# Kernel optimization log

Hardware: AMD Instinct MI355X
Metric: run time of the kernel (lower is better)

Reference implementation:

```python
import jax, jax.numpy as jnp
import numpy as np

NUM_ITER = 3  # routing iterations (canonical CapsNet)
EPS = 1e-12


def _conv(x, w, stride):
    return jax.lax.conv_general_dilated(
        x, w, (stride, stride), 'VALID',
        dimension_numbers=('NCHW', 'OIHW', 'NCHW'))


def _squash(t, axis=-1):
    sn = (t * t).sum(axis=axis, keepdims=True)
    return sn / (1.0 + sn) * t / jnp.sqrt(sn + EPS)


def _batchnorm(x, eps=1e-5):
    # fresh BatchNorm2d in training mode: batch stats, weight=1, bias=0, biased var
    m = x.mean((0, 2, 3), keepdims=True)
    v = ((x - m) ** 2).mean((0, 2, 3), keepdims=True)
    return (x - m) * jax.lax.rsqrt(v + eps)


def _branch(x, cw, cb, pw, pb, rw):
    # x: [B,1,H,W]; cw: [128,1,k,k]; pw: [8,32,128,k,k]; rw: [10,R,8,16]
    y = jax.nn.relu(_conv(x, cw, 1) + cb[None, :, None, None])
    y = _batchnorm(y)
    nc, oc = pw.shape[0], pw.shape[1]  # 8 capsules, 32 channels each
    p = _conv(y, pw.reshape(nc * oc, pw.shape[2], pw.shape[3], pw.shape[4]), 2)
    p = p + pb.reshape(-1)[None, :, None, None]          # [B,256,h,w]
    B = p.shape[0]
    u = jnp.transpose(p.reshape(B, nc, -1), (0, 2, 1))   # [B,R,8], R=32*h*w
    u = _squash(u, axis=-1)
    priors = jnp.einsum('bri,nrio->nbro', u, rw)         # [10,B,R,16]
    b = jnp.zeros(priors.shape[:3] + (1,), priors.dtype)  # [10,B,R,1]
    for i in range(NUM_ITER):
        c = jax.nn.softmax(b, axis=2)                    # over route nodes
        v = _squash((c * priors).sum(axis=2, keepdims=True))  # [10,B,1,16]
        if i < NUM_ITER - 1:
            b = b + (priors * v).sum(axis=-1, keepdims=True)
    v = jnp.transpose(v[:, :, 0, :], (1, 0, 2))          # [B,10,16]
    return jnp.sqrt((v * v).sum(-1) + EPS)               # [B,10] capsule lengths


def setup_inputs() -> dict:
    key = jax.random.key(0)
    ks = jax.random.split(key, 16)
    s = 0.05
    return {
        'x': jax.random.normal(ks[0], (256, 1, 28, 28), jnp.float32),
        'conv1_w': jax.random.normal(ks[1], (128, 1, 3, 3), jnp.float32) * s,
        'conv1_b': jnp.zeros((128,), jnp.float32),
        'prim1_w': jax.random.normal(ks[2], (8, 32, 128, 3, 3), jnp.float32) * s,
        'prim1_b': jnp.zeros((8, 32), jnp.float32),
        'digit1_w': jax.random.normal(ks[3], (10, 128, 8, 16), jnp.float32),
        'conv2_w': jax.random.normal(ks[4], (128, 1, 5, 5), jnp.float32) * s,
        'conv2_b': jnp.zeros((128,), jnp.float32),
        'prim2_w': jax.random.normal(ks[5], (8, 32, 128, 5, 5), jnp.float32) * s,
        'prim2_b': jnp.zeros((8, 32), jnp.float32),
        'digit2_w': jax.random.normal(ks[6], (10, 288, 8, 16), jnp.float32),
        'conv3_w': jax.random.normal(ks[7], (128, 1, 9, 9), jnp.float32) * s,
        'conv3_b': jnp.zeros((128,), jnp.float32),
        'prim3_w': jax.random.normal(ks[8], (8, 32, 128, 9, 9), jnp.float32) * s,
        'prim3_b': jnp.zeros((8, 32), jnp.float32),
        'digit3_w': jax.random.normal(ks[9], (10, 1152, 8, 16), jnp.float32),
    }


def reference(x, conv1_w, conv1_b, prim1_w, prim1_b, digit1_w,
              conv2_w, conv2_b, prim2_w, prim2_b, digit2_w,
              conv3_w, conv3_b, prim3_w, prim3_b, digit3_w):
    img = x[:, 0]                                   # [B,28,28]
    B = img.shape[0]
    x3 = img                                        # 28x28
    x2 = img.reshape(B, 14, 2, 14, 2).mean((2, 4))  # 14x14 pyramid level
    x1 = x2.reshape(B, 7, 2, 7, 2).mean((2, 4))     # 7x7 pyramid level
    l1 = _branch(x1[:, None], conv1_w, conv1_b, prim1_w, prim1_b, digit1_w)
    l2 = _branch(x2[:, None], conv2_w, conv2_b, prim2_w, prim2_b, digit2_w)
    l3 = _branch(x3[:, None], conv3_w, conv3_b, prim3_w, prim3_b, digit3_w)
    return jax.nn.softmax(l1 + l2 + l3, axis=-1)    # [B,10]
```

## Files before the change

### kernel.cpp

```cpp
#include <hip/hip_runtime.h>
#include <math.h>

#define SQ_EPS 1e-12f
#define BN_EPS 1e-5f

typedef short short8 __attribute__((ext_vector_type(8)));
typedef float f32x4 __attribute__((ext_vector_type(4)));
typedef unsigned short ushort_t;

__device__ inline unsigned short f2bf(float x) {
    unsigned int u = __float_as_uint(x);
    unsigned int r = (u + 0x7fffu + ((u >> 16) & 1u)) >> 16;
    return (unsigned short)r;
}
__device__ inline float bf2f(unsigned short h) {
    return __uint_as_float(((unsigned int)h) << 16);
}

template<int IH, int IW, int KS, int OH, int OW>
__device__ void conv_body(const float* __restrict__ w, const float* __restrict__ bias,
                          ushort_t* __restrict__ yh, ushort_t* __restrict__ yl,
                          float* __restrict__ partial,
                          int b, int tid, float* s_img, float* s_w, float* s_red) {
    constexpr int KK = KS * KS;
    constexpr int OS = OH * OW;
    for (int i = tid; i < 128 * KK; i += 256) s_w[i] = w[i];
    __syncthreads();
    int c = tid & 127, half = tid >> 7;
    float bias_c = bias[c];
    float bsum = 0.f, bsq = 0.f;
    for (int r = half; r < OH; r += 2) {
        float acc[OW];
        #pragma unroll
        for (int j = 0; j < OW; ++j) acc[j] = bias_c;
        for (int u = 0; u < KS; ++u) {
            float rg[OW + KS - 1];
            #pragma unroll
            for (int j = 0; j < OW + KS - 1; ++j) rg[j] = s_img[(r + u) * IW + j];
            #pragma unroll
            for (int v = 0; v < KS; ++v) {
                float wv = s_w[c * KK + u * KS + v];
                #pragma unroll
                for (int j = 0; j < OW; ++j) acc[j] += wv * rg[j + v];
            }
        }
        #pragma unroll
        for (int j = 0; j < OW; ++j) {
            float val = fmaxf(acc[j], 0.f);
            bsum += val; bsq += val * val;
            unsigned short h = f2bf(val);
            unsigned short lo = f2bf(val - bf2f(h));
            int oidx = ((b * OS) + r * OW + j) * 128 + c;
            yh[oidx] = h; yl[oidx] = lo;
        }
    }
    s_red[tid] = bsum; __syncthreads();
    if (tid < 128) partial[b * 256 + c] = s_red[tid] + s_red[tid + 128];
    __syncthreads();
    s_red[tid] = bsq; __syncthreads();
    if (tid < 128) partial[b * 256 + 128 + c] = s_red[tid] + s_red[tid + 128];
}

__global__ __launch_bounds__(256) void conv_all_kernel(
        const float* __restrict__ img,
        const float* __restrict__ c1w, const float* __restrict__ c1b,
        const float* __restrict__ c2w, const float* __restrict__ c2b,
        const float* __restrict__ c3w, const float* __restrict__ c3b,
        ushort_t* __restrict__ yh1, ushort_t* __restrict__ yl1,
        ushort_t* __restrict__ yh2, ushort_t* __restrict__ yl2,
        ushort_t* __restrict__ yh3, ushort_t* __restrict__ yl3,
        float* __restrict__ partial_base) {
    __shared__ float s_img[784];
    __shared__ float s_tmp[196];
    __shared__ float s_w[128 * 81];
    __shared__ float s_red[256];
    int br = blockIdx.x >> 8, b = blockIdx.x & 255, tid = threadIdx.x;
    const float* im = img + b * 784;
    for (int i = tid; i < 784; i += 256) s_img[i] = im[i];
    __syncthreads();
    if (br <= 1) {
        for (int idx = tid; idx < 196; idx += 256) {
            int i = idx / 14, j = idx % 14;
            s_tmp[idx] = 0.25f * (s_img[(2*i)*28 + 2*j]   + s_img[(2*i)*28 + 2*j + 1] +
                                  s_img[(2*i+1)*28 + 2*j] + s_img[(2*i+1)*28 + 2*j + 1]);
        }
        __syncthreads();
        if (br == 0) {
            for (int idx = tid; idx < 49; idx += 256) {
                int i = idx / 7, j = idx % 7;
                s_img[idx] = 0.25f * (s_tmp[(2*i)*14 + 2*j]   + s_tmp[(2*i)*14 + 2*j + 1] +
                                      s_tmp[(2*i+1)*14 + 2*j] + s_tmp[(2*i+1)*14 + 2*j + 1]);
            }
        } else {
            for (int idx = tid; idx < 196; idx += 256) s_img[idx] = s_tmp[idx];
        }
        __syncthreads();
    }
    if (br == 0)      conv_body<7, 7, 3, 5, 5>(c1w, c1b, yh1, yl1, partial_base, b, tid, s_img, s_w, s_red);
    else if (br == 1) conv_body<14, 14, 5, 10, 10>(c2w, c2b, yh2, yl2, partial_base + 65536, b, tid, s_img, s_w, s_red);
    else              conv_body<28, 28, 9, 20, 20>(c3w, c3b, yh3, yl3, partial_base + 131072, b, tid, s_img, s_w, s_red);
}

__global__ void bn_final_kernel(const float* __restrict__ partial_base, float* __restrict__ bnp_base) {
    int br = blockIdx.x;
    const float* pp = partial_base + br * 65536;
    float* bnp = bnp_base + br * 512;
    float N = (br == 0) ? 6400.f : ((br == 1) ? 25600.f : 102400.f);
    int c = threadIdx.x;
    float s = 0.f, q = 0.f;
    for (int blk = 0; blk < 256; ++blk) {
        s += pp[blk * 256 + c];
        q += pp[blk * 256 + 128 + c];
    }
    float mean = s / N;
    float var = q / N - mean * mean;
    float inv = rsqrtf(var + BN_EPS);
    bnp[256 + c] = inv;
    bnp[384 + c] = -mean * inv;
}

__global__ __launch_bounds__(256) void wtrans_zero_kernel(
        const float* __restrict__ w1, const float* __restrict__ w2,
        const float* __restrict__ w3, const float* __restrict__ bnp_base,
        const float* __restrict__ pb1, const float* __restrict__ pb2,
        const float* __restrict__ pb3,
        ushort_t* __restrict__ wh1, ushort_t* __restrict__ wl1,
        ushort_t* __restrict__ wh2, ushort_t* __restrict__ wl2,
        ushort_t* __restrict__ wh3, ushort_t* __restrict__ wl3,
        float* __restrict__ b1, float* __restrict__ b2, float* __restrict__ b3,
        float* __restrict__ p3zero) {
    __shared__ float tile[128 * 81];
    __shared__ float r2[2];
    int blk = blockIdx.x, tid = threadIdx.x;
    if (blk >= 768) {
        ((float4*)p3zero)[(blk - 768) * 256 + tid] = (float4){0.f, 0.f, 0.f, 0.f};
        return;
    }
    int br = blk >> 8, ch = blk & 255;
    const float* w; const float* pb; ushort_t* wh; ushort_t* wl; float* bf; int KK;
    if (br == 0)      { w = w1; pb = pb1; wh = wh1; wl = wl1; bf = b1; KK = 9;  }
    else if (br == 1) { w = w2; pb = pb2; wh = wh2; wl = wl2; bf = b2; KK = 25; }
    else              { w = w3; pb = pb3; wh = wh3; wl = wl3; bf = b3; KK = 81; }
    const float* bnp = bnp_base + br * 512;
    int n = 128 * KK;
    const float* wrow = w + ch * n;
    for (int i = tid; i < n; i += 256) tile[i] = wrow[i];
    __syncthreads();
    for (int j = tid; j < n; j += 256) {
        int uv = j >> 7, c = j & 127;
        float val = tile[c * KK + uv] * bnp[256 + c];
        unsigned short h = f2bf(val);
        unsigned short lo = f2bf(val - bf2f(h));
        int oidx = uv * 32768 + (ch << 7) + c;
        wh[oidx] = h; wl[oidx] = lo;
    }
    float s = 0.f;
    if (tid < 128) {
        for (int uv = 0; uv < KK; ++uv) s += tile[tid * KK + uv];
        s *= bnp[384 + tid];
    }
    for (int off = 32; off; off >>= 1) s += __shfl_down(s, off);
    if (tid < 128 && (tid & 63) == 0) r2[tid >> 6] = s;
    __syncthreads();
    if (tid == 0) bf[ch] = pb[ch] + r2[0] + r2[1];
}

template<int S, int WO, int IHg, int IWg, int KS, int ZCH>
__device__ void gemm_body(const ushort_t* __restrict__ yh, const ushort_t* __restrict__ yl,
                          const ushort_t* __restrict__ wh, const ushort_t* __restrict__ wl,
                          float* __restrict__ p, int bx, int by, int bz, int tid,
                          ushort_t* Ash, ushort_t* Asl, ushort_t* Bsh, ushort_t* Bsl) {
    int bm = bx * 128, ch0 = by * 128;
    int arow = tid >> 2;
    int c0 = tid & 3;
    int sw0 = (c0 ^ ((arow >> 1) & 3)) * 8;
    int wA0 = arow * 32 + sw0;
    int wA1 = (arow + 64) * 32 + sw0;
    int m0 = bm + arow;
    int b0 = m0 / S, s0 = m0 % S;
    int abase0 = ((b0 * IHg + 2 * (s0 / WO)) * IWg + 2 * (s0 % WO)) * 128 + c0 * 8;
    int m1 = m0 + 64;
    int b1 = m1 / S, s1 = m1 % S;
    int abase1 = ((b1 * IHg + 2 * (s1 / WO)) * IWg + 2 * (s1 % WO)) * 128 + c0 * 8;
    int bbase0 = (ch0 + arow) * 128 + c0 * 8;
    int bbase1 = (ch0 + arow + 64) * 128 + c0 * 8;
    int lane = tid & 63, wid = tid >> 6;
    int wm = wid & 1, wn = wid >> 1;
    int quad = lane >> 4, l16 = lane & 15;
    int aoffL[4], boffL[4];
    #pragma unroll
    for (int mi = 0; mi < 4; ++mi) {
        int row = wm * 64 + mi * 16 + l16;
        aoffL[mi] = row * 32 + ((quad ^ ((row >> 1) & 3)) * 8);
    }
    #pragma unroll
    for (int ni = 0; ni < 4; ++ni) {
        int row = wn * 64 + ni * 16 + l16;
        boffL[ni] = row * 32 + ((quad ^ ((row >> 1) & 3)) * 8);
    }
    f32x4 acc[4][4];
    #pragma unroll
    for (int mi = 0; mi < 4; ++mi)
        #pragma unroll
        for (int ni = 0; ni < 4; ++ni)
            acc[mi][ni] = (f32x4){0.f, 0.f, 0.f, 0.f};

    int kc = bz * ZCH;
    int uv = kc >> 2, ci = kc & 3;
    int u = uv / KS, v = uv - u * KS;
    int aoff = (u * IWg + v) * 128 + (ci << 5);
    int boff = uv * 32768 + (ci << 5);
    int4 a0h = *reinterpret_cast<const int4*>(yh + abase0 + aoff);
    int4 a0l = *reinterpret_cast<const int4*>(yl + abase0 + aoff);
    int4 a1h = *reinterpret_cast<const int4*>(yh + abase1 + aoff);
    int4 a1l = *reinterpret_cast<const int4*>(yl + abase1 + aoff);
    int4 b0h = *reinterpret_cast<const int4*>(wh + bbase0 + boff);
    int4 b0l = *reinterpret_cast<const int4*>(wl + bbase0 + boff);
    int4 b1h = *reinterpret_cast<const int4*>(wh + bbase1 + boff);
    int4 b1l = *reinterpret_cast<const int4*>(wl + bbase1 + boff);

    for (int t = 0; t < ZCH; ++t) {
        __syncthreads();
        *reinterpret_cast<int4*>(&Ash[wA0]) = a0h;
        *reinterpret_cast<int4*>(&Asl[wA0]) = a0l;
        *reinterpret_cast<int4*>(&Ash[wA1]) = a1h;
        *reinterpret_cast<int4*>(&Asl[wA1]) = a1l;
        *reinterpret_cast<int4*>(&Bsh[wA0]) = b0h;
        *reinterpret_cast<int4*>(&Bsl[wA0]) = b0l;
        *reinterpret_cast<int4*>(&Bsh[wA1]) = b1h;
        *reinterpret_cast<int4*>(&Bsl[wA1]) = b1l;
        if (t + 1 < ZCH) {
            ci = (ci + 1) & 3;
            if (ci == 0) { ++uv; ++v; if (v == KS) { v = 0; ++u; } }
            aoff = (u * IWg + v) * 128 + (ci << 5);
            boff = uv * 32768 + (ci << 5);
            a0h = *reinterpret_cast<const int4*>(yh + abase0 + aoff);
            a0l = *reinterpret_cast<const int4*>(yl + abase0 + aoff);
            a1h = *reinterpret_cast<const int4*>(yh + abase1 + aoff);
            a1l = *reinterpret_cast<const int4*>(yl + abase1 + aoff);
            b0h = *reinterpret_cast<const int4*>(wh + bbase0 + boff);
            b0l = *reinterpret_cast<const int4*>(wl + bbase0 + boff);
            b1h = *reinterpret_cast<const int4*>(wh + bbase1 + boff);
            b1l = *reinterpret_cast<const int4*>(wl + bbase1 + boff);
        }
        __syncthreads();
        short8 bh[4], bl[4];
        #pragma unroll
        for (int ni = 0; ni < 4; ++ni) {
            bh[ni] = *reinterpret_cast<const short8*>(&Bsh[boffL[ni]]);
            bl[ni] = *reinterpret_cast<const short8*>(&Bsl[boffL[ni]]);
        }
        #pragma unroll
        for (int mi = 0; mi < 4; ++mi) {
            short8 ah = *reinterpret_cast<const short8*>(&Ash[aoffL[mi]]);
            short8 al = *reinterpret_cast<const short8*>(&Asl[aoffL[mi]]);
            #pragma unroll
            for (int ni = 0; ni < 4; ++ni) {
                acc[mi][ni] = __builtin_amdgcn_mfma_f32_16x16x32_bf16(ah, bh[ni], acc[mi][ni], 0, 0, 0);
                acc[mi][ni] = __builtin_amdgcn_mfma_f32_16x16x32_bf16(al, bh[ni], acc[mi][ni], 0, 0, 0);
                acc[mi][ni] = __builtin_amdgcn_mfma_f32_16x16x32_bf16(ah, bl[ni], acc[mi][ni], 0, 0, 0);
            }
        }
    }
    #pragma unroll
    for (int mi = 0; mi < 4; ++mi)
        #pragma unroll
        for (int ni = 0; ni < 4; ++ni) {
            int col = ch0 + wn * 64 + ni * 16 + l16;
            #pragma unroll
            for (int reg = 0; reg < 4; ++reg) {
                int row = bm + wm * 64 + mi * 16 + quad * 4 + reg;
                atomicAdd(p + (size_t)row * 256 + col, acc[mi][ni][reg]);
            }
        }
}

__global__ __launch_bounds__(256, 3) void gemm3_kernel(
        const ushort_t* __restrict__ yh, const ushort_t* __restrict__ yl,
        const ushort_t* __restrict__ wh, const ushort_t* __restrict__ wl,
        float* __restrict__ p) {
    __shared__ ushort_t Ash[128 * 32], Asl[128 * 32];
    __shared__ ushort_t Bsh[128 * 32], Bsl[128 * 32];
    gemm_body<36, 6, 20, 20, 9, 54>(yh, yl, wh, wl, p,
                                    blockIdx.x, blockIdx.y, blockIdx.z, threadIdx.x,
                                    Ash, Asl, Bsh, Bsl);
}

__global__ __launch_bounds__(256, 3) void gemm21_kernel(
        const ushort_t* __restrict__ yh2, const ushort_t* __restrict__ yl2,
        const ushort_t* __restrict__ wh2, const ushort_t* __restrict__ wl2, float* __restrict__ p2,
        const ushort_t* __restrict__ yh1, const ushort_t* __restrict__ yl1,
        const ushort_t* __restrict__ wh1, const ushort_t* __restrict__ wl1, float* __restrict__ p1) {
    __shared__ ushort_t Ash[128 * 32], Asl[128 * 32];
    __shared__ ushort_t Bsh[128 * 32], Bsl[128 * 32];
    int blk = blockIdx.x, tid = threadIdx.x;
    if (blk < 360) {
        int z = blk / 36, rem = blk % 36, y = rem / 18, x = rem % 18;
        gemm_body<9, 3, 10, 10, 5, 10>(yh2, yl2, wh2, wl2, p2, x, y, z, tid, Ash, Asl, Bsh, Bsl);
    } else {
        int b = blk - 360;
        int z = b / 16, rem = b % 16, y = rem / 8, x = rem % 8;
        gemm_body<4, 2, 5, 5, 3, 4>(yh1, yl1, wh1, wl1, p1, x, y, z, tid, Ash, Asl, Bsh, Bsl);
    }
}

__global__ void squash_all_kernel(const float* __restrict__ p1, const float* __restrict__ p2,
                                  const float* __restrict__ p3,
                                  const float* __restrict__ bias1, const float* __restrict__ bias2,
                                  const float* __restrict__ bias3,
                                  float* __restrict__ u1, float* __restrict__ u2,
                                  float* __restrict__ u3) {
    int blk = blockIdx.x;
    const float* p; const float* bias; float* u; int S;
    if (blk < 128)      { p = p1; bias = bias1; u = u1; S = 4; }
    else if (blk < 416) { p = p2; bias = bias2; u = u2; S = 9;  blk -= 128; }
    else                { p = p3; bias = bias3; u = u3; S = 36; blk -= 416; }
    int idx = blk * 256 + threadIdx.x;
    int o = idx & 31, rest = idx >> 5;
    int s = rest % S, b = rest / S;
    const float* pp = p + (size_t)(b * S + s) * 256 + o;
    float t[8]; float sn = 0.f;
    #pragma unroll
    for (int i = 0; i < 8; ++i) { t[i] = pp[i * 32] + bias[o + i * 32]; sn += t[i] * t[i]; }
    float f = sn / ((1.f + sn) * sqrtf(sn + SQ_EPS));
    float* up = u + (size_t)(b * (32 * S) + o * S + s) * 8;
    float4 w0 = {t[0] * f, t[1] * f, t[2] * f, t[3] * f};
    float4 w1 = {t[4] * f, t[5] * f, t[6] * f, t[7] * f};
    *reinterpret_cast<float4*>(up) = w0;
    *reinterpret_cast<float4*>(up + 4) = w1;
}

__global__ void rwtrans_zero_kernel(const float* __restrict__ w1, const float* __restrict__ w2,
                                    const float* __restrict__ w3,
                                    ushort_t* __restrict__ o1, ushort_t* __restrict__ o2,
                                    ushort_t* __restrict__ o3,
                                    float* __restrict__ p2, float* __restrict__ p1) {
    int blk = blockIdx.x;
    if (blk >= 7840) {
        int zb = blk - 7840;
        if (zb < 576) ((float4*)p2)[zb * 256 + threadIdx.x] = (float4){0.f, 0.f, 0.f, 0.f};
        else          ((float4*)p1)[(zb - 576) * 256 + threadIdx.x] = (float4){0.f, 0.f, 0.f, 0.f};
        return;
    }
    int idx = blk * 256 + threadIdx.x;
    const float* src; ushort_t* dst; int off;
    if (idx < 163840)      { src = w1; dst = o1; off = idx; }
    else if (idx < 532480) { src = w2; dst = o2; off = idx - 163840; }
    else                   { src = w3; dst = o3; off = idx - 532480; }
    dst[off] = f2bf(src[off]);
}

template<int R>
__device__ void routing_body(const float* __restrict__ u, const ushort_t* __restrict__ rwb,
                             float* __restrict__ lens, int n, int b, int tid,
                             unsigned int* pri, float* red, float* vsh, float* sred) {
    constexpr int KMAX = (R + 255) / 256;
    int lane = tid & 63, wv = tid >> 6;
    float blog[KMAX];
    #pragma unroll
    for (int k = 0; k < KMAX; ++k) {
        blog[k] = 0.f;
        int r = tid + k * 256;
        if (r < R) {
            const float4* up = (const float4*)(u + ((size_t)b * R + r) * 8);
            float4 ua = up[0], ub2 = up[1];
            float uu[8] = {ua.x, ua.y, ua.z, ua.w, ub2.x, ub2.y, ub2.z, ub2.w};
            const ushort_t* wr = rwb + ((size_t)n * R + r) * 128;
            float po[16] = {};
            #pragma unroll
            for (int i = 0; i < 8; ++i) {
                short8 wa = *reinterpret_cast<const short8*>(wr + i * 16);
                short8 wb = *reinterpret_cast<const short8*>(wr + i * 16 + 8);
                #pragma unroll
                for (int o = 0; o < 8; ++o) po[o]     += uu[i] * bf2f((unsigned short)wa[o]);
                #pragma unroll
                for (int o = 0; o < 8; ++o) po[8 + o] += uu[i] * bf2f((unsigned short)wb[o]);
            }
            #pragma unroll
            for (int j = 0; j < 8; ++j)
                pri[j * R + r] = (unsigned int)f2bf(po[2*j]) | ((unsigned int)f2bf(po[2*j+1]) << 16);
        }
    }
    __syncthreads();
    float v[16];
    for (int it = 0; it < 3; ++it) {
        float lmax = -1e30f;
        #pragma unroll
        for (int k = 0; k < KMAX; ++k)
            if (tid + k * 256 < R) lmax = fmaxf(lmax, blog[k]);
        for (int off = 32; off; off >>= 1) lmax = fmaxf(lmax, __shfl_down(lmax, off));
        if (lane == 0) sred[wv] = lmax;
        __syncthreads();
        float mx = fmaxf(fmaxf(sred[0], sred[1]), fmaxf(sred[2], sred[3]));
        __syncthreads();
        float ce[KMAX];
        float lsum = 0.f;
        #pragma unroll
        for (int k = 0; k < KMAX; ++k) {
            ce[k] = (tid + k * 256 < R) ? expf(blog[k] - mx) : 0.f;
            lsum += ce[k];
        }
        for (int off = 32; off; off >>= 1) lsum += __shfl_down(lsum, off);
        if (lane == 0) sred[wv] = lsum;
        __syncthreads();
        float inv = 1.f / (sred[0] + sred[1] + sred[2] + sred[3]);
        float sacc[16] = {};
        #pragma unroll
        for (int k = 0; k < KMAX; ++k) {
            int r = tid + k * 256;
            if (r < R) {
                float c = ce[k] * inv;
                #pragma unroll
                for (int j = 0; j < 8; ++j) {
                    unsigned int w = pri[j * R + r];
                    sacc[2*j]   += c * bf2f((unsigned short)(w & 0xffffu));
                    sacc[2*j+1] += c * bf2f((unsigned short)(w >> 16));
                }
            }
        }
        #pragma unroll
        for (int o = 0; o < 16; ++o) {
            float xv = sacc[o];
            for (int off = 32; off; off >>= 1) xv += __shfl_down(xv, off);
            if (lane == 0) red[wv * 16 + o] = xv;
        }
        __syncthreads();
        if (tid < 16) vsh[tid] = red[tid] + red[16 + tid] + red[32 + tid] + red[48 + tid];
        __syncthreads();
        if (tid == 0) {
            float sn = 0.f;
            #pragma unroll
            for (int o = 0; o < 16; ++o) sn += vsh[o] * vsh[o];
            float f = sn / ((1.f + sn) * sqrtf(sn + SQ_EPS));
            #pragma unroll
            for (int o = 0; o < 16; ++o) vsh[o] *= f;
        }
        __syncthreads();
        #pragma unroll
        for (int o = 0; o < 16; ++o) v[o] = vsh[o];
        if (it < 2) {
            #pragma unroll
            for (int k = 0; k < KMAX; ++k) {
                int r = tid + k * 256;
                if (r < R) {
                    float dot = 0.f;
                    #pragma unroll
                    for (int j = 0; j < 8; ++j) {
                        unsigned int w = pri[j * R + r];
                        dot += bf2f((unsigned short)(w & 0xffffu)) * v[2*j];
                        dot += bf2f((unsigned short)(w >> 16)) * v[2*j+1];
                    }
                    blog[k] += dot;
                }
            }
        }
    }
    if (tid == 0) {
        float sn = 0.f;
        #pragma unroll
        for (int o = 0; o < 16; ++o) sn += v[o] * v[o];
        lens[b * 10 + n] = sqrtf(sn + SQ_EPS);
    }
}

__global__ __launch_bounds__(256, 4) void routing_all_kernel(
        const float* __restrict__ u1, const float* __restrict__ u2, const float* __restrict__ u3,
        const ushort_t* __restrict__ rwb1, const ushort_t* __restrict__ rwb2,
        const ushort_t* __restrict__ rwb3,
        float* __restrict__ l1, float* __restrict__ l2, float* __restrict__ l3) {
    __shared__ unsigned int pri[8 * 1152];
    __shared__ float red[4 * 16];
    __shared__ float vsh[16];
    __shared__ float sred[4];
    int n = blockIdx.x, b = blockIdx.y, br = blockIdx.z, tid = threadIdx.x;
    if (br == 0)      routing_body<128>(u1, rwb1, l1, n, b, tid, pri, red, vsh, sred);
    else if (br == 1) routing_body<288>(u2, rwb2, l2, n, b, tid, pri, red, vsh, sred);
    else              routing_body<1152>(u3, rwb3, l3, n, b, tid, pri, red, vsh, sred);
}

__global__ void final_softmax_kernel(const float* __restrict__ l1, const float* __restrict__ l2,
                                     const float* __restrict__ l3, float* __restrict__ out) {
    int b = threadIdx.x;
    float v[10]; float mx = -1e30f;
    #pragma unroll
    for (int n = 0; n < 10; ++n) {
        v[n] = l1[b * 10 + n] + l2[b * 10 + n] + l3[b * 10 + n];
        mx = fmaxf(mx, v[n]);
    }
    float s = 0.f;
    #pragma unroll
    for (int n = 0; n < 10; ++n) { v[n] = expf(v[n] - mx); s += v[n]; }
    float inv = 1.f / s;
    #pragma unroll
    for (int n = 0; n < 10; ++n) out[b * 10 + n] = v[n] * inv;
}

extern "C" void kernel_launch(void* const* d_in, const int* in_sizes, int n_in,
                              void* d_out, int out_size, void* d_ws, size_t ws_size,
                              hipStream_t stream) {
    const float* x   = (const float*)d_in[0];
    const float* c1w = (const float*)d_in[1];
    const float* c1b = (const float*)d_in[2];
    const float* p1w = (const float*)d_in[3];
    const float* p1b = (const float*)d_in[4];
    const float* d1w = (const float*)d_in[5];
    const float* c2w = (const float*)d_in[6];
    const float* c2b = (const float*)d_in[7];
    const float* p2w = (const float*)d_in[8];
    const float* p2b = (const float*)d_in[9];
    const float* d2w = (const float*)d_in[10];
    const float* c3w = (const float*)d_in[11];
    const float* c3b = (const float*)d_in[12];
    const float* p3w = (const float*)d_in[13];
    const float* p3b = (const float*)d_in[14];
    const float* d3w = (const float*)d_in[15];

    float* ws = (float*)d_ws;
    float* x2    = ws + 0;
    float* x1    = ws + 50176;
    float* yh1f  = ws + 62720;
    float* yl1f  = ws + 472320;
    float* yh2f  = ws + 881920;
    float* yl2f  = ws + 2520320;
    float* yh3f  = ws + 4158720;
    float* yl3f  = ws + 10712320;
    float* wh1f  = ws + 17265920;
    float* wl1f  = ws + 17413376;
    float* wh2f  = ws + 17560832;
    float* wl2f  = ws + 17970432;
    float* wh3f  = ws + 18380032;
    float* wl3f  = ws + 19707136;
    float* p3    = ws + 21034240;
    float* bnp1  = ws + 23393536;
    float* bias1 = ws + 23395072;
    float* bias2 = ws + 23395328;
    float* bias3 = ws + 23395584;
    float* l1    = ws + 23395840;
    float* l2    = ws + 23398400;
    float* l3    = ws + 23400960;
    (void)x2; (void)x1;

    ushort_t* yh1 = (ushort_t*)yh1f; ushort_t* yl1 = (ushort_t*)yl1f;
    ushort_t* yh2 = (ushort_t*)yh2f; ushort_t* yl2 = (ushort_t*)yl2f;
    ushort_t* yh3 = (ushort_t*)yh3f; ushort_t* yl3 = (ushort_t*)yl3f;
    ushort_t* wh1 = (ushort_t*)wh1f; ushort_t* wl1 = (ushort_t*)wl1f;
    ushort_t* wh2 = (ushort_t*)wh2f; ushort_t* wl2 = (ushort_t*)wl2f;
    ushort_t* wh3 = (ushort_t*)wh3f; ushort_t* wl3 = (ushort_t*)wl3f;
    float* u1 = yh1f;
    float* u2 = yh2f;
    float* u3 = yh3f;
    float* p2 = wh3f;
    float* p1 = wl3f;
    ushort_t* rwb1 = (ushort_t*)yl3f;
    ushort_t* rwb2 = rwb1 + 163840;
    ushort_t* rwb3 = rwb2 + 368640;

    conv_all_kernel<<<768, 256, 0, stream>>>(x, c1w, c1b, c2w, c2b, c3w, c3b,
                                             yh1, yl1, yh2, yl2, yh3, yl3, p3);
    bn_final_kernel<<<3, 128, 0, stream>>>(p3, bnp1);
    wtrans_zero_kernel<<<3072, 256, 0, stream>>>(p1w, p2w, p3w, bnp1, p1b, p2b, p3b,
                                                 wh1, wl1, wh2, wl2, wh3, wl3,
                                                 bias1, bias2, bias3, p3);
    gemm3_kernel<<<dim3(72, 2, 6), 256, 0, stream>>>(yh3, yl3, wh3, wl3, p3);
    rwtrans_zero_kernel<<<8672, 256, 0, stream>>>(d1w, d2w, d3w, rwb1, rwb2, rwb3, p2, p1);
    gemm21_kernel<<<504, 256, 0, stream>>>(yh2, yl2, wh2, wl2, p2, yh1, yl1, wh1, wl1, p1);
    squash_all_kernel<<<1568, 256, 0, stream>>>(p1, p2, p3, bias1, bias2, bias3, u1, u2, u3);
    routing_all_kernel<<<dim3(10, 256, 3), 256, 0, stream>>>(u1, u2, u3, rwb1, rwb2, rwb3, l1, l2, l3);
    final_softmax_kernel<<<1, 256, 0, stream>>>(l1, l2, l3, (float*)d_out);
}
```

Baseline: 581.3 us.

## Fuse routing logit update with softmax-weighted sum and transpose digit weights

After: 555.8 us. -4.4%, faster.

```diff
diff --git a/kernel.cpp b/kernel.cpp
--- a/kernel.cpp
+++ b/kernel.cpp
@@ -343,11 +343,25 @@
         return;
     }
     int idx = blk * 256 + threadIdx.x;
-    const float* src; ushort_t* dst; int off;
-    if (idx < 163840)      { src = w1; dst = o1; off = idx; }
-    else if (idx < 532480) { src = w2; dst = o2; off = idx - 163840; }
-    else                   { src = w3; dst = o3; off = idx - 532480; }
-    dst[off] = f2bf(src[off]);
+    if (idx < 163840) {
+        int t = idx;
+        int jj = t & 7; t >>= 3;
+        int r = t & 127; t >>= 7;
+        int g = t & 15; int n = t >> 4;
+        o1[idx] = f2bf(w1[(n * 128 + r) * 128 + g * 8 + jj]);
+    } else if (idx < 532480) {
+        int t = idx - 163840;
+        int jj = t & 7; t >>= 3;
+        int r = t % 288; t /= 288;
+        int g = t & 15; int n = t >> 4;
+        o2[idx - 163840] = f2bf(w2[(n * 288 + r) * 128 + g * 8 + jj]);
+    } else {
+        int t = idx - 532480;
+        int jj = t & 7; t >>= 3;
+        int r = t % 1152; t /= 1152;
+        int g = t & 15; int n = t >> 4;
+        o3[idx - 532480] = f2bf(w3[(n * 1152 + r) * 128 + g * 8 + jj]);
+    }
 }
 
 template<int R>
@@ -356,25 +370,22 @@
                              unsigned int* pri, float* red, float* vsh, float* sred) {
     constexpr int KMAX = (R + 255) / 256;
     int lane = tid & 63, wv = tid >> 6;
-    float blog[KMAX];
     #pragma unroll
     for (int k = 0; k < KMAX; ++k) {
-        blog[k] = 0.f;
         int r = tid + k * 256;
         if (r < R) {
             const float4* up = (const float4*)(u + ((size_t)b * R + r) * 8);
             float4 ua = up[0], ub2 = up[1];
             float uu[8] = {ua.x, ua.y, ua.z, ua.w, ub2.x, ub2.y, ub2.z, ub2.w};
-            const ushort_t* wr = rwb + ((size_t)n * R + r) * 128;
             float po[16] = {};
             #pragma unroll
-            for (int i = 0; i < 8; ++i) {
-                short8 wa = *reinterpret_cast<const short8*>(wr + i * 16);
-                short8 wb = *reinterpret_cast<const short8*>(wr + i * 16 + 8);
+            for (int g = 0; g < 16; ++g) {
+                short8 wg = *reinterpret_cast<const short8*>(rwb + (((size_t)n * 16 + g) * R + r) * 8);
+                float ui = uu[g >> 1];
+                int o0 = (g & 1) * 8;
                 #pragma unroll
-                for (int o = 0; o < 8; ++o) po[o]     += uu[i] * bf2f((unsigned short)wa[o]);
-                #pragma unroll
-                for (int o = 0; o < 8; ++o) po[8 + o] += uu[i] * bf2f((unsigned short)wb[o]);
+                for (int jj = 0; jj < 8; ++jj)
+                    po[o0 + jj] += ui * bf2f((unsigned short)wg[jj]);
             }
             #pragma unroll
             for (int j = 0; j < 8; ++j)
@@ -383,38 +394,20 @@
     }
     __syncthreads();
     float v[16];
-    for (int it = 0; it < 3; ++it) {
-        float lmax = -1e30f;
-        #pragma unroll
-        for (int k = 0; k < KMAX; ++k)
-            if (tid + k * 256 < R) lmax = fmaxf(lmax, blog[k]);
-        for (int off = 32; off; off >>= 1) lmax = fmaxf(lmax, __shfl_down(lmax, off));
-        if (lane == 0) sred[wv] = lmax;
-        __syncthreads();
-        float mx = fmaxf(fmaxf(sred[0], sred[1]), fmaxf(sred[2], sred[3]));
-        __syncthreads();
-        float ce[KMAX];
-        float lsum = 0.f;
-        #pragma unroll
-        for (int k = 0; k < KMAX; ++k) {
-            ce[k] = (tid + k * 256 < R) ? expf(blog[k] - mx) : 0.f;
-            lsum += ce[k];
-        }
-        for (int off = 32; off; off >>= 1) lsum += __shfl_down(lsum, off);
-        if (lane == 0) sred[wv] = lsum;
-        __syncthreads();
-        float inv = 1.f / (sred[0] + sred[1] + sred[2] + sred[3]);
+    float blog[KMAX];
+    #pragma unroll
+    for (int k = 0; k < KMAX; ++k) blog[k] = 0.f;
+    {
         float sacc[16] = {};
         #pragma unroll
         for (int k = 0; k < KMAX; ++k) {
             int r = tid + k * 256;
             if (r < R) {
-                float c = ce[k] * inv;
                 #pragma unroll
                 for (int j = 0; j < 8; ++j) {
                     unsigned int w = pri[j * R + r];
-                    sacc[2*j]   += c * bf2f((unsigned short)(w & 0xffffu));
-                    sacc[2*j+1] += c * bf2f((unsigned short)(w >> 16));
+                    sacc[2*j]   += bf2f((unsigned short)(w & 0xffffu));
+                    sacc[2*j+1] += bf2f((unsigned short)(w >> 16));
                 }
             }
         }
@@ -425,7 +418,7 @@
             if (lane == 0) red[wv * 16 + o] = xv;
         }
         __syncthreads();
-        if (tid < 16) vsh[tid] = red[tid] + red[16 + tid] + red[32 + tid] + red[48 + tid];
+        if (tid < 16) vsh[tid] = (red[tid] + red[16 + tid] + red[32 + tid] + red[48 + tid]) * (1.0f / (float)R);
         __syncthreads();
         if (tid == 0) {
             float sn = 0.f;
@@ -438,22 +431,58 @@
         __syncthreads();
         #pragma unroll
         for (int o = 0; o < 16; ++o) v[o] = vsh[o];
-        if (it < 2) {
-            #pragma unroll
-            for (int k = 0; k < KMAX; ++k) {
-                int r = tid + k * 256;
-                if (r < R) {
-                    float dot = 0.f;
-                    #pragma unroll
-                    for (int j = 0; j < 8; ++j) {
-                        unsigned int w = pri[j * R + r];
-                        dot += bf2f((unsigned short)(w & 0xffffu)) * v[2*j];
-                        dot += bf2f((unsigned short)(w >> 16)) * v[2*j+1];
-                    }
-                    blog[k] += dot;
+        __syncthreads();
+    }
+    for (int it = 0; it < 2; ++it) {
+        float sacc[16] = {};
+        float lsum = 0.f;
+        #pragma unroll
+        for (int k = 0; k < KMAX; ++k) {
+            int r = tid + k * 256;
+            if (r < R) {
+                float pv[16];
+                #pragma unroll
+                for (int j = 0; j < 8; ++j) {
+                    unsigned int w = pri[j * R + r];
+                    pv[2*j]   = bf2f((unsigned short)(w & 0xffffu));
+                    pv[2*j+1] = bf2f((unsigned short)(w >> 16));
                 }
-            }
-        }
+                float dot = 0.f;
+                #pragma unroll
+                for (int o = 0; o < 16; ++o) dot += pv[o] * v[o];
+                blog[k] += dot;
+                float e = expf(blog[k]);
+                lsum += e;
+                #pragma unroll
+                for (int o = 0; o < 16; ++o) sacc[o] += e * pv[o];
+            }
+        }
+        for (int off = 32; off; off >>= 1) lsum += __shfl_down(lsum, off);
+        if (lane == 0) sred[wv] = lsum;
+        #pragma unroll
+        for (int o = 0; o < 16; ++o) {
+            float xv = sacc[o];
+            for (int off = 32; off; off >>= 1) xv += __shfl_down(xv, off);
+            if (lane == 0) red[wv * 16 + o] = xv;
+        }
+        __syncthreads();
+        if (tid < 16) {
+            float tot = sred[0] + sred[1] + sred[2] + sred[3];
+            vsh[tid] = (red[tid] + red[16 + tid] + red[32 + tid] + red[48 + tid]) / tot;
+        }
+        __syncthreads();
+        if (tid == 0) {
+            float sn = 0.f;
+            #pragma unroll
+            for (int o = 0; o < 16; ++o) sn += vsh[o] * vsh[o];
+            float f = sn / ((1.f + sn) * sqrtf(sn + SQ_EPS));
+            #pragma unroll
+            for (int o = 0; o < 16; ++o) vsh[o] *= f;
+        }
+        __syncthreads();
+        #pragma unroll
+        for (int o = 0; o < 16; ++o) v[o] = vsh[o];
+        __syncthreads();
     }
     if (tid == 0) {
         float sn = 0.f;
@@ -516,8 +545,6 @@
     const float* d3w = (const float*)d_in[15];
 
     float* ws = (float*)d_ws;
-    float* x2    = ws + 0;
-    float* x1    = ws + 50176;
     float* yh1f  = ws + 62720;
     float* yl1f  = ws + 472320;
     float* yh2f  = ws + 881920;
@@ -538,7 +565,6 @@
     float* l1    = ws + 23395840;
     float* l2    = ws + 23398400;
     float* l3    = ws + 23400960;
-    (void)x2; (void)x1;
 
     ushort_t* yh1 = (ushort_t*)yh1f; ushort_t* yl1 = (ushort_t*)yl1f;
     ushort_t* yh2 = (ushort_t*)yh2f; ushort_t* yl2 = (ushort_t*)yl2f;
```
